# Kernel optimization log

Hardware: AMD Instinct MI355X
Metric: run time of the kernel (lower is better)

Reference implementation:

```python
import jax, jax.numpy as jnp
import numpy as np

C = 8            # feat_channel
B, K, H, W = 8, 32, 128, 128
CW = (C + 2) * C + C + C * C + C + C + 1  # 169


def setup_inputs() -> dict:
    key = jax.random.key(0)
    k1, k2, k3, k4, k5 = jax.random.split(key, 5)
    seg_feat = jax.random.normal(k1, (B, C, H, W), jnp.float32)
    conv_weight = jax.random.normal(k2, (B, CW, H, W), jnp.float32) * 0.1
    mask = jax.random.randint(k3, (B, K), 0, 2).astype(jnp.int32)
    ind = jax.random.randint(k4, (B, K), 0, H * W).astype(jnp.int64)
    target = jax.random.uniform(k5, (B, K, H, W), jnp.float32)
    return {"seg_feat": seg_feat, "conv_weight": conv_weight, "mask": mask,
            "ind": ind, "target": target}


def reference(seg_feat, conv_weight, mask, ind, target):
    b, c, h, w = seg_feat.shape
    k = ind.shape[1]
    # gather_feature(conv_weight, ind, use_transform=True): [B,CW,H,W] -> [B,HW,CW] -> gather -> [B,K,CW]
    cw = conv_weight.reshape(b, -1, h * w).transpose(0, 2, 1)
    weight = jnp.take_along_axis(cw, ind[:, :, None], axis=1)  # [B,K,CW]

    sizes = [(c + 2) * c, c, c * c, c, c, 1]
    splits = np.cumsum(sizes)[:-1]
    c1w, c1b, c2w, c2b, c3w, c3b = jnp.split(weight, splits, axis=-1)
    c1w = c1w.reshape(b, k, c, c + 2)   # per-object 1x1 conv weights
    c2w = c2w.reshape(b, k, c, c)
    c3w = c3w.reshape(b, k, 1, c)

    x = (ind % w).astype(jnp.float32)
    y = (ind // w).astype(jnp.float32)
    y_grid, x_grid = jnp.meshgrid(jnp.arange(h, dtype=jnp.float32),
                                  jnp.arange(w, dtype=jnp.float32), indexing='ij')
    x_rel = (x_grid[None, None] - x[:, :, None, None]) / w   # [B,K,H,W]
    y_rel = (y_grid[None, None] - y[:, :, None, None]) / h

    feat = jnp.concatenate([
        jnp.broadcast_to(seg_feat[:, None], (b, k, c, h, w)),
        x_rel[:, :, None], y_rel[:, :, None]], axis=2)       # [B,K,C+2,H,W]

    feat = jax.nn.relu(jnp.einsum('bkoc,bkchw->bkohw', c1w, feat) + c1b[..., None, None])
    feat = jax.nn.relu(jnp.einsum('bkoc,bkchw->bkohw', c2w, feat) + c2b[..., None, None])
    pred = jax.nn.sigmoid(jnp.einsum('bkoc,bkchw->bkohw', c3w, feat)
                          + c3b[..., None, None])[:, :, 0]    # [B,K,H,W]

    m = mask.astype(jnp.float32)[:, :, None, None]
    p = pred * m
    t = target * m
    smooth = 1.0
    inter = jnp.sum(p * t, axis=(1, 2, 3))
    denom = jnp.sum(p * p, axis=(1, 2, 3)) + jnp.sum(t * t, axis=(1, 2, 3)) + smooth
    per_img = 1.0 - (2.0 * inter + smooth) / denom
    return jnp.mean(per_img)   # sum over images / valid_batch_size (all valid)
```

## Files before the change

### kernel.cpp

```cpp
#include <hip/hip_runtime.h>

typedef float f32x2 __attribute__((ext_vector_type(2)));

#define C8     8
#define KOBJ   32
#define BIMG   8
#define WW     128
#define HWPIX  16384
#define CWN    169
#define PIX    8
#define GRIDX  8
#define NPAIR  (BIMG * KOBJ)
#define SLOTS_PER_B (KOBJ * GRIDX)
#define NBLK   (NPAIR * GRIDX)

__device__ __forceinline__ void pkfma(f32x2& d, f32x2 a, f32x2 b) {
    asm("v_pk_fma_f32 %0, %1, %2, %0" : "+v"(d) : "v"(a), "v"(b));
}

__global__ __launch_bounds__(256) void mask_head_kernel(
    const float* __restrict__ seg_feat,
    const float* __restrict__ conv_weight,
    const int* __restrict__ mask,
    const long long* __restrict__ ind,
    const float* __restrict__ target,
    float* __restrict__ partial)
{
    const int j    = blockIdx.x;
    const int r    = j >> 3;
    const int tile = j & 7;
    const int t    = threadIdx.x;

    __shared__ f32x2 wd1[C8][10];
    __shared__ f32x2 l1b2[C8];
    __shared__ f32x2 wd2[C8][C8];
    __shared__ f32x2 l2b2[C8];
    __shared__ f32x2 w3d[C8];
    __shared__ float b3s;
    __shared__ float red[4][3];
    __shared__ int   sh_pair, sh_active;

    if (t < 64) {
        const int lane = t;
        const int4 mv = *reinterpret_cast<const int4*>(&mask[lane * 4]);
        const int a0 = (mv.x != 0), a1 = (mv.y != 0), a2 = (mv.z != 0), a3 = (mv.w != 0);
        const int c0 = a0 + a1 + a2 + a3;
        int incl = c0;
#pragma unroll
        for (int off = 1; off < 64; off <<= 1) {
            const int n = __shfl_up(incl, off);
            if (lane >= off) incl += n;
        }
        const int excl  = incl - c0;
        const int total = __shfl(incl, 63);
        const int use_act = (r < total) ? 1 : 0;
        const int rr   = use_act ? r : (r - total);
        const int base = use_act ? excl : (4 * lane - excl);
        const int cnt  = use_act ? c0 : (4 - c0);
        const bool has = (rr >= base) && (rr < base + cnt);
        const int w0 = use_act ? a0 : 1 - a0;
        const int w1 = use_act ? a1 : 1 - a1;
        const int w2 = use_act ? a2 : 1 - a2;
        const int d  = rr - base;
        const int s0 = w0, s1 = w0 + w1, s2 = w0 + w1 + w2;
        const int off4 = (d < s0) ? 0 : (d < s1) ? 1 : (d < s2) ? 2 : 3;
        const int pcand = lane * 4 + off4;
        const unsigned long long bal = __ballot(has);
        const int src = (int)__ffsll((long long)bal) - 1;
        const int pv = __shfl(pcand, src);
        if (lane == 0) { sh_pair = pv; sh_active = use_act; }
    }
    __syncthreads();

    const int pair = sh_pair;
    const int slot = pair * GRIDX + tile;
    if (!sh_active) {
        if (t < 3) partial[slot * 3 + t] = 0.f;
        return;
    }

    const int b = pair >> 5;
    const int idx = (int)ind[pair];

    if (t < CWN) {
        const float v = conv_weight[(b * CWN + t) * HWPIX + idx];
        const f32x2 v2 = {v, v};
        if (t < 80)       { wd1[t / 10][t % 10] = v2; }
        else if (t < 88)  { l1b2[t - 80] = v2; }
        else if (t < 152) { const int u = t - 88; wd2[u >> 3][u & 7] = v2; }
        else if (t < 160) { l2b2[t - 152] = v2; }
        else if (t < 168) { w3d[t - 160] = v2; }
        else              { b3s = v; }
    }
    __syncthreads();

    const float cx = (float)(idx & (WW - 1));
    const float cy = (float)(idx >> 7);

    const float* seg = seg_feat + b * C8 * HWPIX;
    const float* tgt = target + pair * HWPIX;

    const int p0   = tile * 2048 + t * PIX;
    const int row  = p0 >> 7;
    const int col0 = p0 & (WW - 1);
    const float sy = ((float)row - cy) * (1.0f / 128.0f);
    const f32x2 sy2 = {sy, sy};

    const float4 tA = *reinterpret_cast<const float4*>(&tgt[p0]);
    const float4 tB = *reinterpret_cast<const float4*>(&tgt[p0 + 4]);

    float s_pt = 0.f, s_pp = 0.f, s_tt = 0.f;

#pragma unroll
    for (int h = 0; h < 2; ++h) {
        const int q = p0 + h * 4;
        const float colq = (float)(col0 + h * 4);
        const f32x2 sxa = {(colq - cx) * (1.0f / 128.0f),
                           (colq + 1.0f - cx) * (1.0f / 128.0f)};
        const f32x2 sxb = {(colq + 2.0f - cx) * (1.0f / 128.0f),
                           (colq + 3.0f - cx) * (1.0f / 128.0f)};

        f32x2 f2[C8][2];
#pragma unroll
        for (int c = 0; c < C8; ++c) {
            const float4 a = *reinterpret_cast<const float4*>(&seg[c * HWPIX + q]);
            f2[c][0] = {a.x, a.y};
            f2[c][1] = {a.z, a.w};
        }

        f32x2 h1[C8][2];
#pragma unroll
        for (int o = 0; o < C8; ++o) {
            f32x2 base2 = l1b2[o];
            pkfma(base2, wd1[o][9], sy2);
            f32x2 acc0 = base2, acc1 = base2;
            pkfma(acc0, wd1[o][8], sxa);
            pkfma(acc1, wd1[o][8], sxb);
#pragma unroll
            for (int c = 0; c < C8; ++c) {
                const f32x2 w = wd1[o][c];
                pkfma(acc0, w, f2[c][0]);
                pkfma(acc1, w, f2[c][1]);
            }
            h1[o][0] = {fmaxf(acc0.x, 0.f), fmaxf(acc0.y, 0.f)};
            h1[o][1] = {fmaxf(acc1.x, 0.f), fmaxf(acc1.y, 0.f)};
        }

        f32x2 z0 = {b3s, b3s}, z1 = z0;
#pragma unroll
        for (int o = 0; o < C8; ++o) {
            f32x2 acc0 = l2b2[o], acc1 = l2b2[o];
#pragma unroll
            for (int c = 0; c < C8; ++c) {
                const f32x2 w = wd2[o][c];
                pkfma(acc0, w, h1[c][0]);
                pkfma(acc1, w, h1[c][1]);
            }
            const f32x2 r0 = {fmaxf(acc0.x, 0.f), fmaxf(acc0.y, 0.f)};
            const f32x2 r1 = {fmaxf(acc1.x, 0.f), fmaxf(acc1.y, 0.f)};
            const f32x2 w3 = w3d[o];
            pkfma(z0, w3, r0);
            pkfma(z1, w3, r1);
        }

        const float zz[4] = {z0.x, z0.y, z1.x, z1.y};
        const float4 tq = (h == 0) ? tA : tB;
        const float tv[4] = {tq.x, tq.y, tq.z, tq.w};
#pragma unroll
        for (int i = 0; i < 4; ++i) {
            const float e    = __expf(-zz[i]);
            const float pred = __builtin_amdgcn_rcpf(1.0f + e);
            s_pt = fmaf(pred, tv[i], s_pt);
            s_pp = fmaf(pred, pred, s_pp);
            s_tt = fmaf(tv[i], tv[i], s_tt);
        }
    }

#pragma unroll
    for (int off = 32; off > 0; off >>= 1) {
        s_pt += __shfl_down(s_pt, off);
        s_pp += __shfl_down(s_pp, off);
        s_tt += __shfl_down(s_tt, off);
    }
    const int wid = t >> 6;
    if ((t & 63) == 0) { red[wid][0] = s_pt; red[wid][1] = s_pp; red[wid][2] = s_tt; }
    __syncthreads();
    if (t == 0) {
        float a = 0.f, b2 = 0.f, c2 = 0.f;
#pragma unroll
        for (int i = 0; i < 4; ++i) { a += red[i][0]; b2 += red[i][1]; c2 += red[i][2]; }
        partial[slot * 3 + 0] = a;
        partial[slot * 3 + 1] = b2;
        partial[slot * 3 + 2] = c2;
    }
}

__global__ __launch_bounds__(512) void finalize_kernel(
    const float* __restrict__ partial, float* __restrict__ out)
{
    const int t    = threadIdx.x;
    const int b    = t >> 6;
    const int lane = t & 63;

    float pt = 0.f, pp = 0.f, tt = 0.f;
    for (int e = lane; e < SLOTS_PER_B; e += 64) {
        const float* q = partial + (b * SLOTS_PER_B + e) * 3;
        pt += q[0]; pp += q[1]; tt += q[2];
    }
#pragma unroll
    for (int off = 32; off > 0; off >>= 1) {
        pt += __shfl_down(pt, off);
        pp += __shfl_down(pp, off);
        tt += __shfl_down(tt, off);
    }
    __shared__ float per[BIMG];
    if (lane == 0) {
        per[b] = 1.0f - (2.0f * pt + 1.0f) / (pp + tt + 1.0f);
    }
    __syncthreads();
    if (t == 0) {
        float s = 0.f;
#pragma unroll
        for (int i = 0; i < BIMG; ++i) s += per[i];
        out[0] = s * (1.0f / (float)BIMG);
    }
}

extern "C" void kernel_launch(void* const* d_in, const int* in_sizes, int n_in,
                              void* d_out, int out_size, void* d_ws, size_t ws_size,
                              hipStream_t stream) {
    const float*     seg  = (const float*)d_in[0];
    const float*     cw   = (const float*)d_in[1];
    const int*       mask = (const int*)d_in[2];
    const long long* ind  = (const long long*)d_in[3];
    const float*     tgt  = (const float*)d_in[4];
    float* out     = (float*)d_out;
    float* partial = (float*)d_ws;

    mask_head_kernel<<<dim3(NBLK), 256, 0, stream>>>(seg, cw, mask, ind, tgt, partial);
    finalize_kernel<<<1, 512, 0, stream>>>(partial, out);
}
```

Baseline: 21.02 us.

## Drop active-pair compaction scan and prefetch feature loads before the weight barrier

Removes the per-block wavefront prefix scan that remapped block indices so active (masked) pairs were scheduled first. Blocks now index the pair directly from a 3D grid and exit early when the mask is zero. Global loads for the gathered weights, the target and the first half of seg_feat are issued before the shared-memory barrier, and the second half of seg_feat is loaded after the first layer-1 pass, so memory latency overlaps with setup and compute. Without the compaction, inactive blocks are spread across the grid instead of grouped at the end, and holding the prefetched values raises register pressure.

```diff
diff --git a/kernel.cpp b/kernel.cpp
--- a/kernel.cpp
+++ b/kernel.cpp
@@ -10,9 +10,8 @@
 #define CWN    169
 #define PIX    8
 #define GRIDX  8
-#define NPAIR  (BIMG * KOBJ)
 #define SLOTS_PER_B (KOBJ * GRIDX)
-#define NBLK   (NPAIR * GRIDX)
+#define NBLK   (BIMG * KOBJ * GRIDX)
 
 __device__ __forceinline__ void pkfma(f32x2& d, f32x2 a, f32x2 b) {
     asm("v_pk_fma_f32 %0, %1, %2, %0" : "+v"(d) : "v"(a), "v"(b));
@@ -26,10 +25,12 @@
     const float* __restrict__ target,
     float* __restrict__ partial)
 {
-    const int j    = blockIdx.x;
-    const int r    = j >> 3;
-    const int tile = j & 7;
+    const int tile = blockIdx.x;
+    const int k    = blockIdx.y;
+    const int b    = blockIdx.z;
     const int t    = threadIdx.x;
+    const int pair = b * KOBJ + k;
+    const int slot = pair * GRIDX + tile;
 
     __shared__ f32x2 wd1[C8][10];
     __shared__ f32x2 l1b2[C8];
@@ -38,114 +39,79 @@
     __shared__ f32x2 w3d[C8];
     __shared__ float b3s;
     __shared__ float red[4][3];
-    __shared__ int   sh_pair, sh_active;
-
-    if (t < 64) {
-        const int lane = t;
-        const int4 mv = *reinterpret_cast<const int4*>(&mask[lane * 4]);
-        const int a0 = (mv.x != 0), a1 = (mv.y != 0), a2 = (mv.z != 0), a3 = (mv.w != 0);
-        const int c0 = a0 + a1 + a2 + a3;
-        int incl = c0;
-#pragma unroll
-        for (int off = 1; off < 64; off <<= 1) {
-            const int n = __shfl_up(incl, off);
-            if (lane >= off) incl += n;
-        }
-        const int excl  = incl - c0;
-        const int total = __shfl(incl, 63);
-        const int use_act = (r < total) ? 1 : 0;
-        const int rr   = use_act ? r : (r - total);
-        const int base = use_act ? excl : (4 * lane - excl);
-        const int cnt  = use_act ? c0 : (4 - c0);
-        const bool has = (rr >= base) && (rr < base + cnt);
-        const int w0 = use_act ? a0 : 1 - a0;
-        const int w1 = use_act ? a1 : 1 - a1;
-        const int w2 = use_act ? a2 : 1 - a2;
-        const int d  = rr - base;
-        const int s0 = w0, s1 = w0 + w1, s2 = w0 + w1 + w2;
-        const int off4 = (d < s0) ? 0 : (d < s1) ? 1 : (d < s2) ? 2 : 3;
-        const int pcand = lane * 4 + off4;
-        const unsigned long long bal = __ballot(has);
-        const int src = (int)__ffsll((long long)bal) - 1;
-        const int pv = __shfl(pcand, src);
-        if (lane == 0) { sh_pair = pv; sh_active = use_act; }
-    }
-    __syncthreads();
-
-    const int pair = sh_pair;
-    const int slot = pair * GRIDX + tile;
-    if (!sh_active) {
+
+    const int       mval  = mask[pair];
+    const long long idxll = ind[pair];
+    if (mval == 0) {
         if (t < 3) partial[slot * 3 + t] = 0.f;
         return;
     }
-
-    const int b = pair >> 5;
-    const int idx = (int)ind[pair];
+    const int idx = (int)idxll;
+
+    float gv = 0.f;
+    if (t < CWN) gv = conv_weight[(b * CWN + t) * HWPIX + idx];
+
+    const float* seg = seg_feat + b * C8 * HWPIX;
+    const float* tgt = target + pair * HWPIX;
+    const int p0   = tile * 2048 + t * PIX;
+    const int row  = p0 >> 7;
+    const int col0 = p0 & (WW - 1);
+
+    const float4 tA = *reinterpret_cast<const float4*>(&tgt[p0]);
+    const float4 tB = *reinterpret_cast<const float4*>(&tgt[p0 + 4]);
+    float4 s0[C8];
+#pragma unroll
+    for (int c = 0; c < C8; ++c)
+        s0[c] = *reinterpret_cast<const float4*>(&seg[c * HWPIX + p0]);
 
     if (t < CWN) {
-        const float v = conv_weight[(b * CWN + t) * HWPIX + idx];
-        const f32x2 v2 = {v, v};
+        const f32x2 v2 = {gv, gv};
         if (t < 80)       { wd1[t / 10][t % 10] = v2; }
         else if (t < 88)  { l1b2[t - 80] = v2; }
         else if (t < 152) { const int u = t - 88; wd2[u >> 3][u & 7] = v2; }
         else if (t < 160) { l2b2[t - 152] = v2; }
         else if (t < 168) { w3d[t - 160] = v2; }
-        else              { b3s = v; }
+        else              { b3s = gv; }
     }
     __syncthreads();
 
     const float cx = (float)(idx & (WW - 1));
     const float cy = (float)(idx >> 7);
-
-    const float* seg = seg_feat + b * C8 * HWPIX;
-    const float* tgt = target + pair * HWPIX;
-
-    const int p0   = tile * 2048 + t * PIX;
-    const int row  = p0 >> 7;
-    const int col0 = p0 & (WW - 1);
     const float sy = ((float)row - cy) * (1.0f / 128.0f);
     const f32x2 sy2 = {sy, sy};
 
-    const float4 tA = *reinterpret_cast<const float4*>(&tgt[p0]);
-    const float4 tB = *reinterpret_cast<const float4*>(&tgt[p0 + 4]);
-
     float s_pt = 0.f, s_pp = 0.f, s_tt = 0.f;
 
-#pragma unroll
-    for (int h = 0; h < 2; ++h) {
-        const int q = p0 + h * 4;
-        const float colq = (float)(col0 + h * 4);
-        const f32x2 sxa = {(colq - cx) * (1.0f / 128.0f),
-                           (colq + 1.0f - cx) * (1.0f / 128.0f)};
-        const f32x2 sxb = {(colq + 2.0f - cx) * (1.0f / 128.0f),
-                           (colq + 3.0f - cx) * (1.0f / 128.0f)};
-
-        f32x2 f2[C8][2];
+    const float colq0 = (float)col0;
+    f32x2 sxa = {(colq0 - cx) * (1.0f / 128.0f), (colq0 + 1.0f - cx) * (1.0f / 128.0f)};
+    f32x2 sxb = {(colq0 + 2.0f - cx) * (1.0f / 128.0f), (colq0 + 3.0f - cx) * (1.0f / 128.0f)};
+
+    f32x2 h1[C8][2];
+#pragma unroll
+    for (int o = 0; o < C8; ++o) {
+        f32x2 base2 = l1b2[o];
+        pkfma(base2, wd1[o][9], sy2);
+        f32x2 acc0 = base2, acc1 = base2;
+        pkfma(acc0, wd1[o][8], sxa);
+        pkfma(acc1, wd1[o][8], sxb);
 #pragma unroll
         for (int c = 0; c < C8; ++c) {
-            const float4 a = *reinterpret_cast<const float4*>(&seg[c * HWPIX + q]);
-            f2[c][0] = {a.x, a.y};
-            f2[c][1] = {a.z, a.w};
-        }
-
-        f32x2 h1[C8][2];
-#pragma unroll
-        for (int o = 0; o < C8; ++o) {
-            f32x2 base2 = l1b2[o];
-            pkfma(base2, wd1[o][9], sy2);
-            f32x2 acc0 = base2, acc1 = base2;
-            pkfma(acc0, wd1[o][8], sxa);
-            pkfma(acc1, wd1[o][8], sxb);
-#pragma unroll
-            for (int c = 0; c < C8; ++c) {
-                const f32x2 w = wd1[o][c];
-                pkfma(acc0, w, f2[c][0]);
-                pkfma(acc1, w, f2[c][1]);
-            }
-            h1[o][0] = {fmaxf(acc0.x, 0.f), fmaxf(acc0.y, 0.f)};
-            h1[o][1] = {fmaxf(acc1.x, 0.f), fmaxf(acc1.y, 0.f)};
-        }
-
+            const f32x2 w = wd1[o][c];
+            const f32x2 f0 = {s0[c].x, s0[c].y};
+            const f32x2 f1 = {s0[c].z, s0[c].w};
+            pkfma(acc0, w, f0);
+            pkfma(acc1, w, f1);
+        }
+        h1[o][0] = {fmaxf(acc0.x, 0.f), fmaxf(acc0.y, 0.f)};
+        h1[o][1] = {fmaxf(acc1.x, 0.f), fmaxf(acc1.y, 0.f)};
+    }
+
+    float4 s1[C8];
+#pragma unroll
+    for (int c = 0; c < C8; ++c)
+        s1[c] = *reinterpret_cast<const float4*>(&seg[c * HWPIX + p0 + 4]);
+
+    {
         f32x2 z0 = {b3s, b3s}, z1 = z0;
 #pragma unroll
         for (int o = 0; o < C8; ++o) {
@@ -162,10 +128,59 @@
             pkfma(z0, w3, r0);
             pkfma(z1, w3, r1);
         }
-
         const float zz[4] = {z0.x, z0.y, z1.x, z1.y};
-        const float4 tq = (h == 0) ? tA : tB;
-        const float tv[4] = {tq.x, tq.y, tq.z, tq.w};
+        const float tv[4] = {tA.x, tA.y, tA.z, tA.w};
+#pragma unroll
+        for (int i = 0; i < 4; ++i) {
+            const float e    = __expf(-zz[i]);
+            const float pred = __builtin_amdgcn_rcpf(1.0f + e);
+            s_pt = fmaf(pred, tv[i], s_pt);
+            s_pp = fmaf(pred, pred, s_pp);
+            s_tt = fmaf(tv[i], tv[i], s_tt);
+        }
+    }
+
+    const float colq1 = (float)(col0 + 4);
+    sxa = {(colq1 - cx) * (1.0f / 128.0f), (colq1 + 1.0f - cx) * (1.0f / 128.0f)};
+    sxb = {(colq1 + 2.0f - cx) * (1.0f / 128.0f), (colq1 + 3.0f - cx) * (1.0f / 128.0f)};
+
+#pragma unroll
+    for (int o = 0; o < C8; ++o) {
+        f32x2 base2 = l1b2[o];
+        pkfma(base2, wd1[o][9], sy2);
+        f32x2 acc0 = base2, acc1 = base2;
+        pkfma(acc0, wd1[o][8], sxa);
+        pkfma(acc1, wd1[o][8], sxb);
+#pragma unroll
+        for (int c = 0; c < C8; ++c) {
+            const f32x2 w = wd1[o][c];
+            const f32x2 f0 = {s1[c].x, s1[c].y};
+            const f32x2 f1 = {s1[c].z, s1[c].w};
+            pkfma(acc0, w, f0);
+            pkfma(acc1, w, f1);
+        }
+        h1[o][0] = {fmaxf(acc0.x, 0.f), fmaxf(acc0.y, 0.f)};
+        h1[o][1] = {fmaxf(acc1.x, 0.f), fmaxf(acc1.y, 0.f)};
+    }
+    {
+        f32x2 z0 = {b3s, b3s}, z1 = z0;
+#pragma unroll
+        for (int o = 0; o < C8; ++o) {
+            f32x2 acc0 = l2b2[o], acc1 = l2b2[o];
+#pragma unroll
+            for (int c = 0; c < C8; ++c) {
+                const f32x2 w = wd2[o][c];
+                pkfma(acc0, w, h1[c][0]);
+                pkfma(acc1, w, h1[c][1]);
+            }
+            const f32x2 r0 = {fmaxf(acc0.x, 0.f), fmaxf(acc0.y, 0.f)};
+            const f32x2 r1 = {fmaxf(acc1.x, 0.f), fmaxf(acc1.y, 0.f)};
+            const f32x2 w3 = w3d[o];
+            pkfma(z0, w3, r0);
+            pkfma(z1, w3, r1);
+        }
+        const float zz[4] = {z0.x, z0.y, z1.x, z1.y};
+        const float tv[4] = {tB.x, tB.y, tB.z, tB.w};
 #pragma unroll
         for (int i = 0; i < 4; ++i) {
             const float e    = __expf(-zz[i]);
@@ -237,6 +252,7 @@
     float* out     = (float*)d_out;
     float* partial = (float*)d_ws;
 
-    mask_head_kernel<<<dim3(NBLK), 256, 0, stream>>>(seg, cw, mask, ind, tgt, partial);
+    mask_head_kernel<<<dim3(GRIDX, KOBJ, BIMG), 256, 0, stream>>>(
+        seg, cw, mask, ind, tgt, partial);
     finalize_kernel<<<1, 512, 0, stream>>>(partial, out);
 }
```

Measured after the change: 22.22 us. 1.06x slower.
